# Performance work log

Hardware: AMD Instinct MI355X
Metric: run time of the kernel (lower is better)

Reference implementation:

```python
import jax, jax.numpy as jnp
import numpy as np

B = 262144
HIST = 24
FORE = 20
HID = 256
# torch: tau_int = clamp(tau,1,18).long().item(); default tau=6.0 -> static 6 (host sync in torch)
TAU_INT = 6


def setup_inputs() -> dict:
    key = jax.random.key(0)
    ks = jax.random.split(key, 9)
    s = 0.1
    return {
        "history": jax.random.normal(ks[0], (B, HIST), jnp.float32),
        "enc_w1": jax.random.normal(ks[1], (HIST + FORE, HID), jnp.float32) * s,
        "enc_b1": jnp.zeros((HID,), jnp.float32),
        "enc_w2": jax.random.normal(ks[2], (HID, HID), jnp.float32) * s,
        "enc_b2": jnp.zeros((HID,), jnp.float32),
        "cor_w1": jax.random.normal(ks[3], (HID, HID), jnp.float32) * s,
        "cor_b1": jnp.zeros((HID,), jnp.float32),
        "cor_w2": jax.random.normal(ks[4], (HID, FORE), jnp.float32) * s,
        "cor_b2": jnp.zeros((FORE,), jnp.float32),
        "alpha": jnp.float32(0.2),
        "beta": jnp.float32(0.3),
        "gamma": jnp.float32(0.01),
        "tau": jnp.float32(6.0),
        "lambda_mix": jnp.float32(0.5),
    }


def _physics_core(history, alpha, beta, gamma, steps):
    a = jax.nn.sigmoid(alpha)
    b = jax.nn.sigmoid(beta)
    g = jnp.abs(gamma)
    T0 = history[:, -1]                      # [B]
    buf0 = history[:, -TAU_INT:].T           # [tau, B]; buf0[0] = history[:, -tau]

    def step(carry, _):
        T, buf = carry
        T_delayed = buf[0]
        T_new = T - a * T - b * T_delayed - g * T ** 3
        buf = jnp.concatenate([buf[1:], T_new[None, :]], axis=0)
        return (T_new, buf), T_new

    _, preds = jax.lax.scan(step, (T0, buf0), None, length=steps)
    return preds.T                            # [B, steps]


def reference(history, enc_w1, enc_b1, enc_w2, enc_b2,
              cor_w1, cor_b1, cor_w2, cor_b2,
              alpha, beta, gamma, tau, lambda_mix):
    T_physics = _physics_core(history, alpha, beta, gamma, FORE)   # [B, FORE]
    combined = jnp.concatenate([history, T_physics], axis=1)       # [B, HIST+FORE]
    h = jnp.tanh(combined @ enc_w1 + enc_b1)
    features = jnp.tanh(h @ enc_w2 + enc_b2)
    c = jnp.tanh(features @ cor_w1 + cor_b1)
    T_soft = c @ cor_w2 + cor_b2                                   # [B, FORE]
    lam = jax.nn.sigmoid(lambda_mix)
    T_pred = T_physics + lam * T_soft
    return (T_pred, T_physics, T_soft)
```

## Files before the change

kernel.cpp:

```cpp
#include <hip/hip_runtime.h>
#include <hip/hip_bf16.h>

#define NROWS 262144
#define HISTC 24
#define FOREC 20

typedef __bf16        v8bf __attribute__((ext_vector_type(8)));
typedef float         v4f  __attribute__((ext_vector_type(4)));
typedef unsigned int  v4u  __attribute__((ext_vector_type(4)));
typedef unsigned int  v2u  __attribute__((ext_vector_type(2)));

#define WS_WT1_OFF 64
#define WT1_ELEMS 16384
#define WT2_ELEMS 65536
#define WT3_ELEMS 65536
#define WT4_ELEMS 8192

__device__ __forceinline__ unsigned short f2bf(float x) {
    unsigned u = __builtin_bit_cast(unsigned, x);
    u += 0x7FFFu + ((u >> 16) & 1u);
    return (unsigned short)(u >> 16);
}

__device__ __forceinline__ unsigned pack2bf(float a, float b) {
    unsigned ua = __builtin_bit_cast(unsigned, a);
    unsigned ub = __builtin_bit_cast(unsigned, b);
    ua += 0x7FFFu + ((ua >> 16) & 1u);
    ub += 0x7FFFu + ((ub >> 16) & 1u);
    return (ua >> 16) | (ub & 0xFFFF0000u);
}

__device__ __forceinline__ float fast_tanh(float x) {
    float t = x * 2.885390081777927f;
    float p = __builtin_amdgcn_exp2f(t);
    float r = __builtin_amdgcn_rcpf(p + 1.0f);
    return __builtin_fmaf(-2.0f, r, 1.0f);
}

__global__ void prep_kernel(const float* __restrict__ w1, const float* __restrict__ w2,
                            const float* __restrict__ w3, const float* __restrict__ w4,
                            const float* __restrict__ alpha, const float* __restrict__ beta,
                            const float* __restrict__ gamma, const float* __restrict__ lmix,
                            unsigned char* __restrict__ ws)
{
    if (blockIdx.x == 76) {
        int t = threadIdx.x;
        float* wsf = (float*)ws;
        if (t == 0) wsf[0] = 1.0f / (1.0f + expf(-alpha[0]));
        else if (t == 1) wsf[1] = 1.0f / (1.0f + expf(-beta[0]));
        else if (t == 2) wsf[2] = fabsf(gamma[0]);
        else if (t == 3) wsf[3] = 1.0f / (1.0f + expf(-lmix[0]));
        return;
    }
    int idx = (blockIdx.x * 256 + threadIdx.x) * 8;
    const float* src;
    int KT, Kreal, Nreal, srcN, local;
    unsigned short* dst = (unsigned short*)(ws + WS_WT1_OFF);
    if (idx < WT1_ELEMS) {
        local = idx; src = w1; KT = 2; Kreal = 44; Nreal = 256; srcN = 256;
    } else if (idx < WT1_ELEMS + WT2_ELEMS) {
        local = idx - WT1_ELEMS; dst += WT1_ELEMS;
        src = w2; KT = 8; Kreal = 256; Nreal = 256; srcN = 256;
    } else if (idx < WT1_ELEMS + WT2_ELEMS + WT3_ELEMS) {
        local = idx - (WT1_ELEMS + WT2_ELEMS); dst += WT1_ELEMS + WT2_ELEMS;
        src = w3; KT = 8; Kreal = 256; Nreal = 256; srcN = 256;
    } else {
        local = idx - (WT1_ELEMS + WT2_ELEMS + WT3_ELEMS);
        dst += WT1_ELEMS + WT2_ELEMS + WT3_ELEMS;
        src = w4; KT = 8; Kreal = 256; Nreal = 20; srcN = 20;
    }
    int L   = (local >> 3) & 63;
    int blk = local >> 9;
    int kt = blk % KT, nt = blk / KT;
    int cc = L & 15,  qq = L >> 4;
    int feat = nt * 16 + cc;
    int kbase = kt * 32 + qq * 8;
    unsigned short tmp[8];
#pragma unroll
    for (int j = 0; j < 8; ++j) {
        int k = kbase + j;
        float v = (k < Kreal && feat < Nreal) ? src[k * srcN + feat] : 0.0f;
        tmp[j] = f2bf(v);
    }
    v4u pk;
    pk[0] = tmp[0] | ((unsigned)tmp[1] << 16);
    pk[1] = tmp[2] | ((unsigned)tmp[3] << 16);
    pk[2] = tmp[4] | ((unsigned)tmp[5] << 16);
    pk[3] = tmp[6] | ((unsigned)tmp[7] << 16);
    *(v4u*)&dst[local] = pk;
}

template<int KT, int SIN>
__device__ __forceinline__ void layer123(unsigned short* buf,
        const unsigned short* __restrict__ wsw, const float* __restrict__ bias,
        int w, int c, int q, int lane)
{
    const v4u* wp = (const v4u*)wsw;
    v4f acc[2][4];
#pragma unroll
    for (int ft = 0; ft < 2; ++ft)
#pragma unroll
        for (int st = 0; st < 4; ++st) {
            v4f z = {0.0f, 0.0f, 0.0f, 0.0f};
            acc[ft][st] = z;
        }

#pragma unroll 2
    for (int kt = 0; kt < KT; ++kt) {
        v4u a0 = wp[((w * 2 + 0) * KT + kt) * 64 + lane];
        v4u a1 = wp[((w * 2 + 1) * KT + kt) * 64 + lane];
#pragma unroll
        for (int st = 0; st < 4; ++st) {
            v4u braw = *(const v4u*)&buf[(st * 16 + c) * SIN + kt * 32 + q * 8];
            v8bf bb = __builtin_bit_cast(v8bf, braw);
            acc[0][st] = __builtin_amdgcn_mfma_f32_16x16x32_bf16(
                __builtin_bit_cast(v8bf, a0), bb, acc[0][st], 0, 0, 0);
            acc[1][st] = __builtin_amdgcn_mfma_f32_16x16x32_bf16(
                __builtin_bit_cast(v8bf, a1), bb, acc[1][st], 0, 0, 0);
        }
    }

    __syncthreads();

#pragma unroll
    for (int ft = 0; ft < 2; ++ft) {
        v4f bi = *(const v4f*)&bias[w * 32 + ft * 16 + q * 4];
#pragma unroll
        for (int st = 0; st < 4; ++st) {
            float x0 = fast_tanh(acc[ft][st][0] + bi[0]);
            float x1 = fast_tanh(acc[ft][st][1] + bi[1]);
            float x2 = fast_tanh(acc[ft][st][2] + bi[2]);
            float x3 = fast_tanh(acc[ft][st][3] + bi[3]);
            v2u d; d[0] = pack2bf(x0, x1); d[1] = pack2bf(x2, x3);
            *(v2u*)&buf[(st * 16 + c) * 264 + w * 32 + ft * 16 + q * 4] = d;
        }
    }
    __syncthreads();
}

__global__ __launch_bounds__(512, 4) void fused_kernel(
    const float* __restrict__ history,
    const float* __restrict__ eb1, const float* __restrict__ eb2,
    const float* __restrict__ cb1, const float* __restrict__ cb2,
    const unsigned char* __restrict__ ws, float* __restrict__ out)
{
    __shared__ unsigned short buf[64 * 264];
    __shared__ float tp[64 * 20];

    const int tid  = threadIdx.x;
    const int w    = tid >> 6;
    const int lane = tid & 63;
    const int c    = lane & 15;
    const int q    = lane >> 4;
    const int row0 = blockIdx.x << 6;
    const float* wsf = (const float*)ws;
    const unsigned short* wt1 = (const unsigned short*)(ws + WS_WT1_OFF);
    const unsigned short* wt2 = wt1 + WT1_ELEMS;
    const unsigned short* wt3 = wt2 + WT2_ELEMS;
    const unsigned short* wt4 = wt3 + WT3_ELEMS;

    float* hist = (float*)&buf[8192];

#pragma unroll
    for (int i = 0; i < 3; ++i) {
        int e = tid + i * 512;
        int r = e / 24, cc = e - r * 24;
        hist[r * 25 + cc] = history[row0 * 24 + e];
    }
    __syncthreads();

#pragma unroll
    for (int i = 0; i < 3; ++i) {
        int e = tid + i * 512;
        int r = e / 24, cc = e - r * 24;
        buf[r * 72 + cc] = f2bf(hist[r * 25 + cc]);
    }
#pragma unroll
    for (int i = 0; i < 3; ++i) {
        int e = tid + i * 512;
        if (e < 1280) {
            int r = e / 20, cc = e - r * 20;
            buf[r * 72 + 44 + cc] = 0;
        }
    }
    if (tid < 64) {
        float pa = wsf[0], pb = wsf[1], pg = wsf[2];
        float d0 = hist[tid * 25 + 18], d1 = hist[tid * 25 + 19], d2 = hist[tid * 25 + 20];
        float d3 = hist[tid * 25 + 21], d4 = hist[tid * 25 + 22], d5 = hist[tid * 25 + 23];
        float T = d5;
#pragma unroll
        for (int s = 0; s < 20; ++s) {
            float t3 = T * T * T;
            float Tn = T - pa * T;
            Tn = Tn - pb * d0;
            Tn = Tn - pg * t3;
            tp[tid * 20 + s] = Tn;
            buf[tid * 72 + 24 + s] = f2bf(Tn);
            d0 = d1; d1 = d2; d2 = d3; d3 = d4; d4 = d5; d5 = Tn;
            T = Tn;
        }
    }
    __syncthreads();

    layer123<2, 72>(buf, wt1, eb1, w, c, q, lane);
    layer123<8, 264>(buf, wt2, eb2, w, c, q, lane);
    layer123<8, 264>(buf, wt3, cb1, w, c, q, lane);

    const int ft4 = w >> 2;
    const int st4 = w & 3;
    const v4u* wp4 = (const v4u*)wt4;
    v4f acc4 = {0.0f, 0.0f, 0.0f, 0.0f};
#pragma unroll 2
    for (int kt = 0; kt < 8; ++kt) {
        v4u a = wp4[(ft4 * 8 + kt) * 64 + lane];
        v4u braw = *(const v4u*)&buf[(st4 * 16 + c) * 264 + kt * 32 + q * 8];
        v8bf bb = __builtin_bit_cast(v8bf, braw);
        acc4 = __builtin_amdgcn_mfma_f32_16x16x32_bf16(
            __builtin_bit_cast(v8bf, a), bb, acc4, 0, 0, 0);
    }

    const float lam = wsf[3];
    const long sample = (long)row0 + st4 * 16 + c;
    float* outP = out;
    float* outF = out + (long)NROWS * 20;
    float* outS = out + (long)NROWS * 40;
    const int f0 = ft4 * 16 + q * 4;
    if (f0 < 20) {
        v4f bi  = *(const v4f*)&cb2[f0];
        v4f tph = *(const v4f*)&tp[(st4 * 16 + c) * 20 + f0];
        v4f ts, pr;
#pragma unroll
        for (int r = 0; r < 4; ++r) {
            ts[r] = acc4[r] + bi[r];
            pr[r] = tph[r] + lam * ts[r];
        }
        *(v4f*)&outS[sample * 20 + f0] = ts;
        *(v4f*)&outP[sample * 20 + f0] = pr;
        *(v4f*)&outF[sample * 20 + f0] = tph;
    }
}

extern "C" void kernel_launch(void* const* d_in, const int* in_sizes, int n_in,
                              void* d_out, int out_size, void* d_ws, size_t ws_size,
                              hipStream_t stream)
{
    const float* history = (const float*)d_in[0];
    const float* enc_w1  = (const float*)d_in[1];
    const float* enc_b1  = (const float*)d_in[2];
    const float* enc_w2  = (const float*)d_in[3];
    const float* enc_b2  = (const float*)d_in[4];
    const float* cor_w1  = (const float*)d_in[5];
    const float* cor_b1  = (const float*)d_in[6];
    const float* cor_w2  = (const float*)d_in[7];
    const float* cor_b2  = (const float*)d_in[8];
    const float* alpha   = (const float*)d_in[9];
    const float* beta    = (const float*)d_in[10];
    const float* gamma   = (const float*)d_in[11];
    const float* lmix    = (const float*)d_in[13];

    prep_kernel<<<77, 256, 0, stream>>>(enc_w1, enc_w2, cor_w1, cor_w2,
                                        alpha, beta, gamma, lmix,
                                        (unsigned char*)d_ws);
    fused_kernel<<<NROWS / 64, 512, 0, stream>>>(history, enc_b1, enc_b2, cor_b1, cor_b2,
                                                 (const unsigned char*)d_ws, (float*)d_out);
}
```

Before: 216.6 us.

## Halve block to 4 waves with 64 features per wave and vectorized history load

Each block now runs 256 threads (4 waves) instead of 512, and each wave computes 64 output features per layer instead of 32. Every B-fragment read from LDS therefore feeds four MFMAs instead of two, which halves LDS traffic per MFMA. The history tile is loaded with float4 reads and converted straight into the padded 264-stride LDS buffer, and the physics recurrence reads its seed values from global memory, so the fp32 staging pass and one barrier are gone. The cost is twice the accumulator registers per wave (64 floats), which may lower occupancy, and fewer waves in flight to hide latency.

```diff
diff --git a/kernel.cpp b/kernel.cpp
--- a/kernel.cpp
+++ b/kernel.cpp
@@ -7,6 +7,7 @@
 
 typedef __bf16        v8bf __attribute__((ext_vector_type(8)));
 typedef float         v4f  __attribute__((ext_vector_type(4)));
+typedef float         v2f  __attribute__((ext_vector_type(2)));
 typedef unsigned int  v4u  __attribute__((ext_vector_type(4)));
 typedef unsigned int  v2u  __attribute__((ext_vector_type(2)));
 
@@ -90,15 +91,15 @@
     *(v4u*)&dst[local] = pk;
 }
 
-template<int KT, int SIN>
+template<int KT>
 __device__ __forceinline__ void layer123(unsigned short* buf,
         const unsigned short* __restrict__ wsw, const float* __restrict__ bias,
         int w, int c, int q, int lane)
 {
     const v4u* wp = (const v4u*)wsw;
-    v4f acc[2][4];
-#pragma unroll
-    for (int ft = 0; ft < 2; ++ft)
+    v4f acc[4][4];
+#pragma unroll
+    for (int ft = 0; ft < 4; ++ft)
 #pragma unroll
         for (int st = 0; st < 4; ++st) {
             v4f z = {0.0f, 0.0f, 0.0f, 0.0f};
@@ -107,24 +108,26 @@
 
 #pragma unroll 2
     for (int kt = 0; kt < KT; ++kt) {
-        v4u a0 = wp[((w * 2 + 0) * KT + kt) * 64 + lane];
-        v4u a1 = wp[((w * 2 + 1) * KT + kt) * 64 + lane];
+        v4u a[4];
+#pragma unroll
+        for (int ft = 0; ft < 4; ++ft)
+            a[ft] = wp[((w * 4 + ft) * KT + kt) * 64 + lane];
 #pragma unroll
         for (int st = 0; st < 4; ++st) {
-            v4u braw = *(const v4u*)&buf[(st * 16 + c) * SIN + kt * 32 + q * 8];
+            v4u braw = *(const v4u*)&buf[(st * 16 + c) * 264 + kt * 32 + q * 8];
             v8bf bb = __builtin_bit_cast(v8bf, braw);
-            acc[0][st] = __builtin_amdgcn_mfma_f32_16x16x32_bf16(
-                __builtin_bit_cast(v8bf, a0), bb, acc[0][st], 0, 0, 0);
-            acc[1][st] = __builtin_amdgcn_mfma_f32_16x16x32_bf16(
-                __builtin_bit_cast(v8bf, a1), bb, acc[1][st], 0, 0, 0);
+#pragma unroll
+            for (int ft = 0; ft < 4; ++ft)
+                acc[ft][st] = __builtin_amdgcn_mfma_f32_16x16x32_bf16(
+                    __builtin_bit_cast(v8bf, a[ft]), bb, acc[ft][st], 0, 0, 0);
         }
     }
 
     __syncthreads();
 
 #pragma unroll
-    for (int ft = 0; ft < 2; ++ft) {
-        v4f bi = *(const v4f*)&bias[w * 32 + ft * 16 + q * 4];
+    for (int ft = 0; ft < 4; ++ft) {
+        v4f bi = *(const v4f*)&bias[w * 64 + ft * 16 + q * 4];
 #pragma unroll
         for (int st = 0; st < 4; ++st) {
             float x0 = fast_tanh(acc[ft][st][0] + bi[0]);
@@ -132,13 +135,13 @@
             float x2 = fast_tanh(acc[ft][st][2] + bi[2]);
             float x3 = fast_tanh(acc[ft][st][3] + bi[3]);
             v2u d; d[0] = pack2bf(x0, x1); d[1] = pack2bf(x2, x3);
-            *(v2u*)&buf[(st * 16 + c) * 264 + w * 32 + ft * 16 + q * 4] = d;
+            *(v2u*)&buf[(st * 16 + c) * 264 + w * 64 + ft * 16 + q * 4] = d;
         }
     }
     __syncthreads();
 }
 
-__global__ __launch_bounds__(512, 4) void fused_kernel(
+__global__ __launch_bounds__(256, 4) void fused_kernel(
     const float* __restrict__ history,
     const float* __restrict__ eb1, const float* __restrict__ eb2,
     const float* __restrict__ cb1, const float* __restrict__ cb2,
@@ -159,34 +162,32 @@
     const unsigned short* wt3 = wt2 + WT2_ELEMS;
     const unsigned short* wt4 = wt3 + WT3_ELEMS;
 
-    float* hist = (float*)&buf[8192];
-
-#pragma unroll
-    for (int i = 0; i < 3; ++i) {
-        int e = tid + i * 512;
-        int r = e / 24, cc = e - r * 24;
-        hist[r * 25 + cc] = history[row0 * 24 + e];
-    }
-    __syncthreads();
-
-#pragma unroll
-    for (int i = 0; i < 3; ++i) {
-        int e = tid + i * 512;
-        int r = e / 24, cc = e - r * 24;
-        buf[r * 72 + cc] = f2bf(hist[r * 25 + cc]);
-    }
-#pragma unroll
-    for (int i = 0; i < 3; ++i) {
-        int e = tid + i * 512;
-        if (e < 1280) {
-            int r = e / 20, cc = e - r * 20;
-            buf[r * 72 + 44 + cc] = 0;
+#pragma unroll
+    for (int i = 0; i < 2; ++i) {
+        int e = tid + i * 256;
+        if (e < 384) {
+            int r  = e / 6, c4 = e - r * 6;
+            v4f h4 = *(const v4f*)&history[(long)(row0 + r) * 24 + c4 * 4];
+            v2u d; d[0] = pack2bf(h4[0], h4[1]); d[1] = pack2bf(h4[2], h4[3]);
+            *(v2u*)&buf[r * 264 + c4 * 4] = d;
+        }
+    }
+#pragma unroll
+    for (int i = 0; i < 2; ++i) {
+        int e = tid + i * 256;
+        if (e < 320) {
+            int r = e / 5, g = e - r * 5;
+            v2u z = {0u, 0u};
+            *(v2u*)&buf[r * 264 + 44 + g * 4] = z;
         }
     }
     if (tid < 64) {
+        const float* hrow = &history[(long)(row0 + tid) * 24];
+        v2f h18 = *(const v2f*)&hrow[18];
+        v4f h20 = *(const v4f*)&hrow[20];
         float pa = wsf[0], pb = wsf[1], pg = wsf[2];
-        float d0 = hist[tid * 25 + 18], d1 = hist[tid * 25 + 19], d2 = hist[tid * 25 + 20];
-        float d3 = hist[tid * 25 + 21], d4 = hist[tid * 25 + 22], d5 = hist[tid * 25 + 23];
+        float d0 = h18[0], d1 = h18[1], d2 = h20[0];
+        float d3 = h20[1], d4 = h20[2], d5 = h20[3];
         float T = d5;
 #pragma unroll
         for (int s = 0; s < 20; ++s) {
@@ -195,48 +196,62 @@
             Tn = Tn - pb * d0;
             Tn = Tn - pg * t3;
             tp[tid * 20 + s] = Tn;
-            buf[tid * 72 + 24 + s] = f2bf(Tn);
+            buf[tid * 264 + 24 + s] = f2bf(Tn);
             d0 = d1; d1 = d2; d2 = d3; d3 = d4; d4 = d5; d5 = Tn;
             T = Tn;
         }
     }
     __syncthreads();
 
-    layer123<2, 72>(buf, wt1, eb1, w, c, q, lane);
-    layer123<8, 264>(buf, wt2, eb2, w, c, q, lane);
-    layer123<8, 264>(buf, wt3, cb1, w, c, q, lane);
-
-    const int ft4 = w >> 2;
-    const int st4 = w & 3;
+    layer123<2>(buf, wt1, eb1, w, c, q, lane);
+    layer123<8>(buf, wt2, eb2, w, c, q, lane);
+    layer123<8>(buf, wt3, cb1, w, c, q, lane);
+
     const v4u* wp4 = (const v4u*)wt4;
-    v4f acc4 = {0.0f, 0.0f, 0.0f, 0.0f};
+    v4f acc40 = {0.0f, 0.0f, 0.0f, 0.0f}, acc41 = {0.0f, 0.0f, 0.0f, 0.0f};
 #pragma unroll 2
     for (int kt = 0; kt < 8; ++kt) {
-        v4u a = wp4[(ft4 * 8 + kt) * 64 + lane];
-        v4u braw = *(const v4u*)&buf[(st4 * 16 + c) * 264 + kt * 32 + q * 8];
+        v4u a0 = wp4[(0 * 8 + kt) * 64 + lane];
+        v4u a1 = wp4[(1 * 8 + kt) * 64 + lane];
+        v4u braw = *(const v4u*)&buf[(w * 16 + c) * 264 + kt * 32 + q * 8];
         v8bf bb = __builtin_bit_cast(v8bf, braw);
-        acc4 = __builtin_amdgcn_mfma_f32_16x16x32_bf16(
-            __builtin_bit_cast(v8bf, a), bb, acc4, 0, 0, 0);
+        acc40 = __builtin_amdgcn_mfma_f32_16x16x32_bf16(
+            __builtin_bit_cast(v8bf, a0), bb, acc40, 0, 0, 0);
+        acc41 = __builtin_amdgcn_mfma_f32_16x16x32_bf16(
+            __builtin_bit_cast(v8bf, a1), bb, acc41, 0, 0, 0);
     }
 
     const float lam = wsf[3];
-    const long sample = (long)row0 + st4 * 16 + c;
+    const long sample = (long)row0 + w * 16 + c;
     float* outP = out;
     float* outF = out + (long)NROWS * 20;
     float* outS = out + (long)NROWS * 40;
-    const int f0 = ft4 * 16 + q * 4;
-    if (f0 < 20) {
+    {
+        int f0 = q * 4;
         v4f bi  = *(const v4f*)&cb2[f0];
-        v4f tph = *(const v4f*)&tp[(st4 * 16 + c) * 20 + f0];
+        v4f tph = *(const v4f*)&tp[(w * 16 + c) * 20 + f0];
         v4f ts, pr;
 #pragma unroll
         for (int r = 0; r < 4; ++r) {
-            ts[r] = acc4[r] + bi[r];
+            ts[r] = acc40[r] + bi[r];
             pr[r] = tph[r] + lam * ts[r];
         }
         *(v4f*)&outS[sample * 20 + f0] = ts;
         *(v4f*)&outP[sample * 20 + f0] = pr;
         *(v4f*)&outF[sample * 20 + f0] = tph;
+    }
+    if (q == 0) {
+        v4f bi  = *(const v4f*)&cb2[16];
+        v4f tph = *(const v4f*)&tp[(w * 16 + c) * 20 + 16];
+        v4f ts, pr;
+#pragma unroll
+        for (int r = 0; r < 4; ++r) {
+            ts[r] = acc41[r] + bi[r];
+            pr[r] = tph[r] + lam * ts[r];
+        }
+        *(v4f*)&outS[sample * 20 + 16] = ts;
+        *(v4f*)&outP[sample * 20 + 16] = pr;
+        *(v4f*)&outF[sample * 20 + 16] = tph;
     }
 }
 
@@ -261,6 +276,6 @@
     prep_kernel<<<77, 256, 0, stream>>>(enc_w1, enc_w2, cor_w1, cor_w2,
                                         alpha, beta, gamma, lmix,
                                         (unsigned char*)d_ws);
-    fused_kernel<<<NROWS / 64, 512, 0, stream>>>(history, enc_b1, enc_b2, cor_b1, cor_b2,
+    fused_kernel<<<NROWS / 64, 256, 0, stream>>>(history, enc_b1, enc_b2, cor_b1, cor_b2,
                                                  (const unsigned char*)d_ws, (float*)d_out);
 }
```

After: 210.9 us. 1.03x faster.
